# Optimization experiments

Hardware: AMD Instinct MI355X
Metric: run time of the kernel (lower is better)

Reference implementation:

```python
import jax, jax.numpy as jnp
import numpy as np

D_MODEL = 1024
D_STATE = 16
D_CONV = 4
EXPAND = 1
D_INNER = EXPAND * D_MODEL  # must equal D_MODEL for original dt_proj shapes to work
BATCH = 2
SEQ = 2048


def silu(x):
    return x * jax.nn.sigmoid(x)


def setup_inputs() -> dict:
    key = jax.random.key(0)
    ks = jax.random.split(key, 8)
    s = 0.02
    return {
        "x": jax.random.normal(ks[0], (BATCH, SEQ, D_MODEL), dtype=jnp.float32),
        "W_in": jax.random.normal(ks[1], (2 * D_INNER, D_MODEL), dtype=jnp.float32) * s,
        "conv_w": jax.random.normal(ks[2], (D_INNER, D_CONV), dtype=jnp.float32) * s,
        "conv_b": jnp.zeros((D_INNER,), dtype=jnp.float32),
        "W_dt": jax.random.normal(ks[3], (D_INNER, D_INNER), dtype=jnp.float32) * s,
        "b_dt": jnp.zeros((D_INNER,), dtype=jnp.float32),
        "A_log": jnp.zeros((D_INNER, D_STATE), dtype=jnp.float32),  # torch: log(ones)=0
        "Bp": jax.random.normal(ks[4], (D_INNER, D_STATE), dtype=jnp.float32),
        "Cp": jax.random.normal(ks[5], (D_INNER, D_STATE), dtype=jnp.float32),
        "Dp": jnp.ones((D_INNER,), dtype=jnp.float32),
        "W_out": jax.random.normal(ks[6], (D_MODEL, D_INNER), dtype=jnp.float32) * s,
    }


def reference(x, W_in, conv_w, conv_b, W_dt, b_dt, A_log, Bp, Cp, Dp, W_out):
    B, L, _ = x.shape
    # in_proj then split into ssm branch and gating residual
    xr = x @ W_in.T                               # (B, L, 2*D_INNER)
    x_proj, res = jnp.split(xr, 2, axis=-1)       # each (B, L, D_INNER)

    # causal depthwise conv1d (kernel D_CONV), == torch conv1d(padding=K-1)[..., :L]
    xp = jnp.pad(x_proj, ((0, 0), (D_CONV - 1, 0), (0, 0)))
    xc = conv_b + sum(conv_w[:, k] * xp[:, k:k + L, :] for k in range(D_CONV))
    xc = silu(xc)                                 # (B, L, D_INNER)

    # selective SSM scan
    delta = jax.nn.softplus(xc @ W_dt.T + b_dt)   # (B, L, D_INNER)
    A = -jnp.exp(A_log)                           # (D_INNER, D_STATE)
    dA = jnp.exp(delta[..., None] * A)            # (B, L, D_INNER, D_STATE)
    dBx = delta[..., None] * Bp * xc[..., None]   # (B, L, D_INNER, D_STATE)

    def step(h, inp):
        dA_t, dBx_t = inp                         # (B, D_INNER, D_STATE)
        h = dA_t * h + dBx_t
        y = jnp.einsum('bdn,dn->bd', h, Cp)
        return h, y

    h0 = jnp.zeros((B, D_INNER, D_STATE), dtype=x.dtype)
    _, ys = jax.lax.scan(step, h0, (dA.transpose(1, 0, 2, 3), dBx.transpose(1, 0, 2, 3)))
    x_ssm = ys.transpose(1, 0, 2) + xc * Dp       # (B, L, D_INNER)

    return (x_ssm * silu(res)) @ W_out.T          # (B, L, D_MODEL)
```

## Files before the change

### kernel.cpp

```cpp
#include <hip/hip_runtime.h>

typedef unsigned short u16;
typedef __bf16 bf16;
typedef bf16 bf16x8 __attribute__((ext_vector_type(8)));
typedef float f32x4 __attribute__((ext_vector_type(4)));

#define SEQ     2048
#define BATCH   2
#define DM      1024
#define DI      1024
#define NROW    (BATCH*SEQ)
#define NSTATE  16
#define NCHUNK  64
#define CLEN    32

static_assert(SEQ == NCHUNK * CLEN, "chunking must cover SEQ");

__device__ __forceinline__ u16 f2bf(float f) {
  unsigned u = __builtin_bit_cast(unsigned, f);
  u += 0x7FFFu + ((u >> 16) & 1u);
  return (u16)(u >> 16);
}
__device__ __forceinline__ float sigm(float x) { return 1.f / (1.f + __expf(-x)); }

__global__ __launch_bounds__(256) void k_cvt_all(
    const float* __restrict__ x, const float* __restrict__ Win,
    const float* __restrict__ Wdt, const float* __restrict__ Wout,
    u16* __restrict__ xbf, u16* __restrict__ winbf,
    u16* __restrict__ wdtbf, u16* __restrict__ woutbf)
{
  long i = (long)blockIdx.x * 256 + threadIdx.x;
  const float* src; u16* dst; long off;
  if (i < 1048576)            { src = x;    dst = xbf;    off = i; }
  else if (i < 1572864)       { src = Win;  dst = winbf;  off = i - 1048576; }
  else if (i < 1835008)       { src = Wdt;  dst = wdtbf;  off = i - 1572864; }
  else                        { src = Wout; dst = woutbf; off = i - 1835008; }
  float4 v = reinterpret_cast<const float4*>(src)[off];
  ushort4 o;
  o.x = f2bf(v.x); o.y = f2bf(v.y); o.z = f2bf(v.z); o.w = f2bf(v.w);
  reinterpret_cast<ushort4*>(dst)[off] = o;
}

#define BM 128
#define BK 32

__device__ __forceinline__ void gload16(const u16* g, u16* l) {
  __builtin_amdgcn_global_load_lds((const __attribute__((address_space(1))) void*)g,
                                   (__attribute__((address_space(3))) void*)l,
                                   16, 0, 0);
}

template<int EPI, int BN>
__global__ __launch_bounds__(256) void k_gemm(
    const u16* __restrict__ A, const u16* __restrict__ B,
    float* __restrict__ out0, float* __restrict__ out1,
    const float* __restrict__ bias, int M, int N, int K)
{
  __shared__ __align__(16) u16 sA[2 * BM * BK];
  __shared__ __align__(16) u16 sB[2 * BN * BK];
  const int t = threadIdx.x;
  const int wave = t >> 6, lane = t & 63;
  const int lr = lane & 15, kb = lane >> 4;
  const int wr = wave >> 1, wc = wave & 1;
  const long bm = (long)blockIdx.y * BM, bn = (long)blockIdx.x * BN;

  f32x4 acc[4][BN / 32] = {};

  const int srow = t >> 2;
  const int scol = (t & 3) * 8;
  const u16* gA0 = A + (bm + srow) * (long)K + scol;
  const u16* gB0 = B + (bn + srow) * (long)K + scol;

  auto STAGE = [&](int buf, int k0) {
    #pragma unroll
    for (int i = 0; i < BM / 64; ++i)
      gload16(gA0 + (long)i * 64 * K + k0,
              &sA[buf * (BM * BK) + i * (64 * BK) + wave * 512]);
    #pragma unroll
    for (int i = 0; i < BN / 64; ++i)
      gload16(gB0 + (long)i * 64 * K + k0,
              &sB[buf * (BN * BK) + i * (64 * BK) + wave * 512]);
  };

  STAGE(0, 0);
  __syncthreads();
  int cur = 0;
  for (int k0 = 0; k0 < K; k0 += BK) {
    if (k0 + BK < K) STAGE(cur ^ 1, k0 + BK);
    const u16* pa = &sA[cur * (BM * BK) + (wr * 64 + lr) * BK + kb * 8];
    const u16* pb = &sB[cur * (BN * BK) + (wc * (BN / 2) + lr) * BK + kb * 8];
    bf16x8 af[4], bfr[BN / 32];
    #pragma unroll
    for (int mi = 0; mi < 4; ++mi)
      af[mi] = *reinterpret_cast<const bf16x8*>(pa + mi * 16 * BK);
    #pragma unroll
    for (int ni = 0; ni < BN / 32; ++ni)
      bfr[ni] = *reinterpret_cast<const bf16x8*>(pb + ni * 16 * BK);
    #pragma unroll
    for (int mi = 0; mi < 4; ++mi)
      #pragma unroll
      for (int ni = 0; ni < BN / 32; ++ni)
        acc[mi][ni] = __builtin_amdgcn_mfma_f32_16x16x32_bf16(af[mi], bfr[ni], acc[mi][ni], 0, 0, 0);
    __syncthreads();
    cur ^= 1;
  }

  #pragma unroll
  for (int mi = 0; mi < 4; ++mi) {
    const long row0 = bm + wr * 64 + mi * 16 + kb * 4;
    #pragma unroll
    for (int ni = 0; ni < BN / 32; ++ni) {
      const long col = bn + wc * (BN / 2) + ni * 16 + lr;
      #pragma unroll
      for (int j = 0; j < 4; ++j) {
        const float v = acc[mi][ni][j];
        const long r = row0 + j;
        if (EPI == 0) {
          out0[r * N + col] = v;
        } else if (EPI == 1) {
          if (col < DI) out0[r * DI + col] = v;
          else          out1[r * DI + (col - DI)] = v * sigm(v);
        } else {
          float z = v + bias[col];
          out0[r * N + col] = fmaxf(z, 0.f) + log1pf(__expf(-fabsf(z)));
        }
      }
    }
  }
}

__global__ void k_conv(const float* __restrict__ xproj, const float* __restrict__ convw,
                       const float* __restrict__ convb, float* __restrict__ xc,
                       u16* __restrict__ xcbf)
{
  const int idx = blockIdx.x * 256 + threadIdx.x;
  const int d = idx & (DI - 1);
  const int m = idx >> 10;
  const int l = m & (SEQ - 1);
  float acc = convb[d];
  #pragma unroll
  for (int k = 0; k < 4; ++k) {
    int ls = l + k - 3;
    if (ls >= 0)
      acc = fmaf(convw[d * 4 + k], xproj[(long)(m + k - 3) * DI + d], acc);
  }
  float s = acc * sigm(acc);
  xc[idx] = s;
  xcbf[idx] = f2bf(s);
}

__global__ __launch_bounds__(256) void k_scanA(
    const float* __restrict__ delta, const float* __restrict__ xc,
    const float* __restrict__ A_log, const float* __restrict__ Bp,
    float* __restrict__ hfin, float* __restrict__ sumdt_buf)
{
  const int tid = threadIdx.x, blk = blockIdx.x;
  const int d = (blk & 3) * 256 + tid;
  const int c = (blk >> 2) & (NCHUNK - 1);
  const int b = blk >> 8;
  float Aa[NSTATE], Bb[NSTATE], h[NSTATE];
  #pragma unroll
  for (int n = 0; n < NSTATE; ++n) {
    Aa[n] = -__expf(A_log[d * NSTATE + n]);
    Bb[n] = Bp[d * NSTATE + n];
    h[n] = 0.f;
  }
  const long base = ((long)(b * SEQ + c * CLEN)) * DI + d;
  float sdt = 0.f;
  for (int i = 0; i < CLEN; ++i) {
    float dt = delta[base + (long)i * DI];
    float x  = xc[base + (long)i * DI];
    sdt += dt;
    float dx = dt * x;
    #pragma unroll
    for (int n = 0; n < NSTATE; ++n) {
      float da = __expf(dt * Aa[n]);
      h[n] = fmaf(da, h[n], dx * Bb[n]);
    }
  }
  const long sb = ((long)(b * NCHUNK + c) * NSTATE) * DI + d;
  #pragma unroll
  for (int n = 0; n < NSTATE; ++n) hfin[sb + (long)n * DI] = h[n];
  sumdt_buf[(long)(b * NCHUNK + c) * DI + d] = sdt;
}

__global__ __launch_bounds__(256) void k_combine(
    const float* __restrict__ hfin, const float* __restrict__ sumdt_buf,
    const float* __restrict__ A_log, float* __restrict__ hstart)
{
  const int idx = blockIdx.x * 256 + threadIdx.x;
  const int d = idx & (DI - 1);
  const int n = (idx >> 10) & (NSTATE - 1);
  const int b = idx >> 14;
  const float Aa = -__expf(A_log[d * NSTATE + n]);
  float h = 0.f;
  for (int c = 0; c < NCHUNK; ++c) {
    const long sb = ((long)(b * NCHUNK + c) * NSTATE + n) * DI + d;
    hstart[sb] = h;
    float sdt = sumdt_buf[(long)(b * NCHUNK + c) * DI + d];
    h = fmaf(__expf(Aa * sdt), h, hfin[sb]);
  }
}

__global__ __launch_bounds__(256) void k_scanB(
    const float* __restrict__ delta, const float* __restrict__ xc,
    const float* __restrict__ A_log, const float* __restrict__ Bp,
    const float* __restrict__ Cp, const float* __restrict__ Dp,
    const float* __restrict__ sres, const float* __restrict__ hstart,
    u16* __restrict__ gated)
{
  const int tid = threadIdx.x, blk = blockIdx.x;
  const int d = (blk & 3) * 256 + tid;
  const int c = (blk >> 2) & (NCHUNK - 1);
  const int b = blk >> 8;
  float Aa[NSTATE], Bb[NSTATE], Cc[NSTATE], h[NSTATE];
  #pragma unroll
  for (int n = 0; n < NSTATE; ++n) {
    Aa[n] = -__expf(A_log[d * NSTATE + n]);
    Bb[n] = Bp[d * NSTATE + n];
    Cc[n] = Cp[d * NSTATE + n];
  }
  const float Dd = Dp[d];
  const long sb = ((long)(b * NCHUNK + c) * NSTATE) * DI + d;
  #pragma unroll
  for (int n = 0; n < NSTATE; ++n) h[n] = hstart[sb + (long)n * DI];
  const long base = ((long)(b * SEQ + c * CLEN)) * DI + d;
  for (int i = 0; i < CLEN; ++i) {
    float dt = delta[base + (long)i * DI];
    float x  = xc[base + (long)i * DI];
    float dx = dt * x;
    float y = 0.f;
    #pragma unroll
    for (int n = 0; n < NSTATE; ++n) {
      float da = __expf(dt * Aa[n]);
      h[n] = fmaf(da, h[n], dx * Bb[n]);
      y = fmaf(h[n], Cc[n], y);
    }
    float xs = fmaf(x, Dd, y);
    float g = xs * sres[base + (long)i * DI];
    gated[base + (long)i * DI] = f2bf(g);
  }
}

extern "C" void kernel_launch(void* const* d_in, const int* in_sizes, int n_in,
                              void* d_out, int out_size, void* d_ws, size_t ws_size,
                              hipStream_t stream)
{
  const float* x      = (const float*)d_in[0];
  const float* W_in   = (const float*)d_in[1];
  const float* conv_w = (const float*)d_in[2];
  const float* conv_b = (const float*)d_in[3];
  const float* W_dt   = (const float*)d_in[4];
  const float* b_dt   = (const float*)d_in[5];
  const float* A_log  = (const float*)d_in[6];
  const float* Bp     = (const float*)d_in[7];
  const float* Cp     = (const float*)d_in[8];
  const float* Dp     = (const float*)d_in[9];
  const float* W_out  = (const float*)d_in[10];
  float* out = (float*)d_out;

  const long MD = (long)NROW * DI;

  char* ws = (char*)d_ws;
  float* silu_res = (float*)ws;             ws += MD * 4;
  float* xc_f32   = (float*)ws;             ws += MD * 4;
  float* delta    = (float*)ws;             ws += MD * 4;
  u16*   xc_bf    = (u16*)ws;               ws += MD * 2;
  u16*   xbf      = (u16*)ws;               ws += MD * 2;
  u16*   Win_bf   = (u16*)ws;               ws += (long)2 * DI * DM * 2;
  u16*   Wdt_bf   = (u16*)ws;               ws += (long)DI * DI * 2;
  u16*   Wout_bf  = (u16*)ws;               ws += (long)DM * DI * 2;
  float* hfin     = (float*)ws;             ws += (long)BATCH * NCHUNK * NSTATE * DI * 4;
  float* sumdt    = (float*)ws;             ws += (long)BATCH * NCHUNK * DI * 4;
  float* hstart   = (float*)ws;             ws += (long)BATCH * NCHUNK * NSTATE * DI * 4;

  float* x_proj = delta;
  u16*   gated  = xbf;

  k_cvt_all<<<dim3(8192), dim3(256), 0, stream>>>(
      x, W_in, W_dt, W_out, xbf, Win_bf, Wdt_bf, Wout_bf);

  k_gemm<1, 128><<<dim3(2 * DI / 128, NROW / BM), dim3(256), 0, stream>>>(
      xbf, Win_bf, x_proj, silu_res, nullptr, NROW, 2 * DI, DM);

  k_conv<<<dim3((unsigned)(MD / 256)), dim3(256), 0, stream>>>(x_proj, conv_w, conv_b, xc_f32, xc_bf);

  k_gemm<2, 64><<<dim3(DI / 64, NROW / BM), dim3(256), 0, stream>>>(
      xc_bf, Wdt_bf, delta, nullptr, b_dt, NROW, DI, DI);

  k_scanA<<<dim3(BATCH * NCHUNK * (DI / 256)), dim3(256), 0, stream>>>(
      delta, xc_f32, A_log, Bp, hfin, sumdt);
  k_combine<<<dim3(BATCH * NSTATE * DI / 256), dim3(256), 0, stream>>>(
      hfin, sumdt, A_log, hstart);
  k_scanB<<<dim3(BATCH * NCHUNK * (DI / 256)), dim3(256), 0, stream>>>(
      delta, xc_f32, A_log, Bp, Cp, Dp, silu_res, hstart, gated);

  k_gemm<0, 64><<<dim3(DM / 64, NROW / BM), dim3(256), 0, stream>>>(
      gated, Wout_bf, out, nullptr, nullptr, NROW, DM, DI);
}
```

Measured before the change: 175.3 us.

## Retile GEMMs to smaller blocks with XCD-aware 1D grid remapping

```diff
diff --git a/kernel.cpp b/kernel.cpp
--- a/kernel.cpp
+++ b/kernel.cpp
@@ -13,6 +13,7 @@
 #define NSTATE  16
 #define NCHUNK  64
 #define CLEN    32
+#define BK      32
 
 static_assert(SEQ == NCHUNK * CLEN, "chunking must cover SEQ");
 
@@ -41,8 +42,6 @@
   reinterpret_cast<ushort4*>(dst)[off] = o;
 }
 
-#define BM 128
-#define BK 32
 
 __device__ __forceinline__ void gload16(const u16* g, u16* l) {
   __builtin_amdgcn_global_load_lds((const __attribute__((address_space(1))) void*)g,
@@ -50,21 +49,28 @@
                                    16, 0, 0);
 }
 
-template<int EPI, int BN>
-__global__ __launch_bounds__(256) void k_gemm(
+template<int EPI, int BM, int BN, int GX>
+__global__ __launch_bounds__(256, 4) void k_gemm(
     const u16* __restrict__ A, const u16* __restrict__ B,
     float* __restrict__ out0, float* __restrict__ out1,
     const float* __restrict__ bias, int M, int N, int K)
 {
+  constexpr int MI_ = BM / 32;
+  constexpr int NI_ = BN / 32;
   __shared__ __align__(16) u16 sA[2 * BM * BK];
   __shared__ __align__(16) u16 sB[2 * BN * BK];
   const int t = threadIdx.x;
   const int wave = t >> 6, lane = t & 63;
   const int lr = lane & 15, kb = lane >> 4;
   const int wr = wave >> 1, wc = wave & 1;
-  const long bm = (long)blockIdx.y * BM, bn = (long)blockIdx.x * BN;
-
-  f32x4 acc[4][BN / 32] = {};
+
+  const int nwg = gridDim.x;
+  const int bid = blockIdx.x;
+  const int wg  = (bid & 7) * (nwg >> 3) + (bid >> 3);
+  const long bm = (long)(wg / GX) * BM;
+  const long bn = (long)(wg % GX) * BN;
+
+  f32x4 acc[MI_][NI_] = {};
 
   const int srow = t >> 2;
   const int scol = (t & 3) * 8;
@@ -87,29 +93,29 @@
   int cur = 0;
   for (int k0 = 0; k0 < K; k0 += BK) {
     if (k0 + BK < K) STAGE(cur ^ 1, k0 + BK);
-    const u16* pa = &sA[cur * (BM * BK) + (wr * 64 + lr) * BK + kb * 8];
+    const u16* pa = &sA[cur * (BM * BK) + (wr * (BM / 2) + lr) * BK + kb * 8];
     const u16* pb = &sB[cur * (BN * BK) + (wc * (BN / 2) + lr) * BK + kb * 8];
-    bf16x8 af[4], bfr[BN / 32];
-    #pragma unroll
-    for (int mi = 0; mi < 4; ++mi)
+    bf16x8 af[MI_], bfr[NI_];
+    #pragma unroll
+    for (int mi = 0; mi < MI_; ++mi)
       af[mi] = *reinterpret_cast<const bf16x8*>(pa + mi * 16 * BK);
     #pragma unroll
-    for (int ni = 0; ni < BN / 32; ++ni)
+    for (int ni = 0; ni < NI_; ++ni)
       bfr[ni] = *reinterpret_cast<const bf16x8*>(pb + ni * 16 * BK);
     #pragma unroll
-    for (int mi = 0; mi < 4; ++mi)
+    for (int mi = 0; mi < MI_; ++mi)
       #pragma unroll
-      for (int ni = 0; ni < BN / 32; ++ni)
+      for (int ni = 0; ni < NI_; ++ni)
         acc[mi][ni] = __builtin_amdgcn_mfma_f32_16x16x32_bf16(af[mi], bfr[ni], acc[mi][ni], 0, 0, 0);
     __syncthreads();
     cur ^= 1;
   }
 
   #pragma unroll
-  for (int mi = 0; mi < 4; ++mi) {
-    const long row0 = bm + wr * 64 + mi * 16 + kb * 4;
-    #pragma unroll
-    for (int ni = 0; ni < BN / 32; ++ni) {
+  for (int mi = 0; mi < MI_; ++mi) {
+    const long row0 = bm + wr * (BM / 2) + mi * 16 + kb * 4;
+    #pragma unroll
+    for (int ni = 0; ni < NI_; ++ni) {
       const long col = bn + wc * (BN / 2) + ni * 16 + lr;
       #pragma unroll
       for (int j = 0; j < 4; ++j) {
@@ -280,12 +286,12 @@
   k_cvt_all<<<dim3(8192), dim3(256), 0, stream>>>(
       x, W_in, W_dt, W_out, xbf, Win_bf, Wdt_bf, Wout_bf);
 
-  k_gemm<1, 128><<<dim3(2 * DI / 128, NROW / BM), dim3(256), 0, stream>>>(
+  k_gemm<1, 128, 64, 32><<<dim3(1024), dim3(256), 0, stream>>>(
       xbf, Win_bf, x_proj, silu_res, nullptr, NROW, 2 * DI, DM);
 
   k_conv<<<dim3((unsigned)(MD / 256)), dim3(256), 0, stream>>>(x_proj, conv_w, conv_b, xc_f32, xc_bf);
 
-  k_gemm<2, 64><<<dim3(DI / 64, NROW / BM), dim3(256), 0, stream>>>(
+  k_gemm<2, 64, 64, 16><<<dim3(1024), dim3(256), 0, stream>>>(
       xc_bf, Wdt_bf, delta, nullptr, b_dt, NROW, DI, DI);
 
   k_scanA<<<dim3(BATCH * NCHUNK * (DI / 256)), dim3(256), 0, stream>>>(
@@ -295,6 +301,6 @@
   k_scanB<<<dim3(BATCH * NCHUNK * (DI / 256)), dim3(256), 0, stream>>>(
       delta, xc_f32, A_log, Bp, Cp, Dp, silu_res, hstart, gated);
 
-  k_gemm<0, 64><<<dim3(DM / 64, NROW / BM), dim3(256), 0, stream>>>(
+  k_gemm<0, 64, 64, 16><<<dim3(1024), dim3(256), 0, stream>>>(
       gated, Wout_bf, out, nullptr, nullptr, NROW, DM, DI);
 }
```

After: 168.2 us. -4.1%, faster.
